# Kernel tuning notes

Hardware: AMD Instinct MI355X
Metric: run time of the kernel (lower is better)

The kernel has to match this reference:

```python
import jax, jax.numpy as jnp
import numpy as np

C, D, H, Z, B = 10, 3072, 512, 256, 2048  # classes, img_dim, hidden, latent, batch


def setup_inputs() -> dict:
    key = jax.random.key(0)
    ks = jax.random.split(key, 8)
    def w(k, shape, fan_in):
        return jax.random.normal(k, shape, jnp.float32) * (1.0 / np.sqrt(fan_in)).astype(np.float32)
    return {
        "img": jax.random.normal(ks[0], (B, D), jnp.float32),
        "label": jax.random.randint(ks[1], (B,), 0, C, dtype=jnp.int32),
        "enc_w1": w(ks[2], (C, D, H), D), "enc_b1": jnp.zeros((C, H), jnp.float32),
        "enc_w2": w(ks[3], (C, H, Z), H), "enc_b2": jnp.zeros((C, Z), jnp.float32),
        "dec_w1": w(ks[4], (C, Z, H), Z), "dec_b1": jnp.zeros((C, H), jnp.float32),
        "dec_w2": w(ks[5], (C, H, D), H), "dec_b2": jnp.zeros((C, D), jnp.float32),
    }


def reference(img, label, enc_w1, enc_b1, enc_w2, enc_b2,
              dec_w1, dec_b1, dec_w2, dec_b2):
    # Label-conditioned dispatch: rows with label==c go through expert c's
    # encoder-decoder; outputs scattered back into a zero-initialized image.
    # Loop is over a small fixed class count (structurally distinct experts);
    # masked-select via jnp.where is mathematically identical to the
    # gather/scatter in the torch code (absent classes contribute nothing).
    out_img = jnp.zeros_like(img)
    n_classes = enc_w1.shape[0]
    for c in range(n_classes):
        h = jax.nn.relu(img @ enc_w1[c] + enc_b1[c])       # [B,H]
        z = h @ enc_w2[c] + enc_b2[c]                      # [B,Z] latent code
        h2 = jax.nn.relu(z @ dec_w1[c] + dec_b1[c])        # [B,H]
        y = h2 @ dec_w2[c] + dec_b2[c]                     # [B,D]
        out_img = jnp.where((label == c)[:, None], y, out_img)
    loss = jnp.mean((out_img - img) ** 2)
    return loss, out_img
```

## Files before the change

kernel.cpp:

```cpp
#include <hip/hip_runtime.h>
#include <hip/hip_bf16.h>

#define C_CLS 10
#define DIM   3072
#define HID   512
#define LAT   256
#define BATCH 2048
#define BM    64
#define GRID_TILES 42

typedef __attribute__((ext_vector_type(8))) short  s16x8;
typedef __attribute__((ext_vector_type(4))) short  s16x4;
typedef __attribute__((ext_vector_type(4))) float  f32x4;
typedef __attribute__((ext_vector_type(8))) __bf16 bf16x8;

struct Meta {
    int offsets[C_CLS + 1];
    int ntiles;
    int tileClass[GRID_TILES];
    int tileRow[GRID_TILES];
    int perm[BATCH];
};

__device__ __forceinline__ unsigned short f2bf(float f) {
    unsigned u = __builtin_bit_cast(unsigned, f);
    unsigned r = (u + 0x7fffu + ((u >> 16) & 1u)) >> 16;
    return (unsigned short)r;
}

__device__ __forceinline__ f32x4 mfma16(s16x8 a, s16x8 b, f32x4 c) {
    return __builtin_amdgcn_mfma_f32_16x16x32_bf16(
        __builtin_bit_cast(bf16x8, a), __builtin_bit_cast(bf16x8, b), c, 0, 0, 0);
}

__global__ __launch_bounds__(256) void setup_kernel(const int* __restrict__ label,
                                                    Meta* __restrict__ mt,
                                                    float* __restrict__ out) {
    __shared__ int h[C_CLS];
    __shared__ int loff[C_CLS + 1];
    int tid = threadIdx.x;
    if (tid < C_CLS) h[tid] = 0;
    __syncthreads();
    for (int i = tid; i < BATCH; i += 256) atomicAdd(&h[label[i]], 1);
    __syncthreads();
    if (tid == 0) {
        int s = 0, nt = 0;
        for (int c = 0; c < C_CLS; ++c) { loff[c] = s; s += h[c]; }
        loff[C_CLS] = s;
        for (int c = 0; c < C_CLS; ++c) {
            mt->offsets[c] = loff[c];
            int cnt = h[c];
            for (int t = 0; t < cnt; t += BM) {
                mt->tileClass[nt] = c;
                mt->tileRow[nt]   = loff[c] + t;
                ++nt;
            }
            h[c] = loff[c];
        }
        mt->offsets[C_CLS] = loff[C_CLS];
        mt->ntiles = nt;
        out[0] = 0.0f;
    }
    __syncthreads();
    for (int i = tid; i < BATCH; i += 256) {
        int pos = atomicAdd(&h[label[i]], 1);
        mt->perm[pos] = i;
    }
}

__global__ __launch_bounds__(256) void gather_kernel(const float* __restrict__ img,
                                                     const Meta* __restrict__ mt,
                                                     unsigned short* __restrict__ Xg) {
    int p    = blockIdx.x;
    int orig = mt->perm[p];
    const float4* src = (const float4*)(img + (size_t)orig * DIM);
    unsigned short* dst = Xg + (size_t)p * DIM;
    for (int j = threadIdx.x; j < DIM / 4; j += 256) {
        float4 v = src[j];
        s16x4 o;
        o.x = (short)f2bf(v.x); o.y = (short)f2bf(v.y);
        o.z = (short)f2bf(v.z); o.w = (short)f2bf(v.w);
        *(s16x4*)(dst + 4 * j) = o;
    }
}

__global__ __launch_bounds__(256) void transpose_cvt(const float* __restrict__ src,
                                                     unsigned short* __restrict__ dst,
                                                     int K, int N) {
    __shared__ unsigned short tile[32][33];
    int c  = blockIdx.z;
    int n0 = blockIdx.x * 32, k0 = blockIdx.y * 32;
    src += (size_t)c * K * N;
    dst += (size_t)c * N * K;
    int tx = threadIdx.x, ty = threadIdx.y;
#pragma unroll
    for (int i = 0; i < 4; ++i) {
        int k = k0 + ty + i * 8;
        tile[ty + i * 8][tx] = f2bf(src[(size_t)k * N + n0 + tx]);
    }
    __syncthreads();
#pragma unroll
    for (int i = 0; i < 4; ++i) {
        int n = n0 + ty + i * 8;
        dst[(size_t)n * K + k0 + tx] = tile[tx][ty + i * 8];
    }
}

template <int K, int N, bool RELU, bool FINAL>
__global__ __launch_bounds__(256) void gemm_kernel(const unsigned short* __restrict__ A,
                                                   const unsigned short* __restrict__ Wt,
                                                   const float* __restrict__ bias,
                                                   unsigned short* __restrict__ Aout,
                                                   float* __restrict__ outF,
                                                   const float* __restrict__ img,
                                                   const Meta* __restrict__ mt) {
    int ty = blockIdx.y;
    if (ty >= mt->ntiles) return;
    const int c    = mt->tileClass[ty];
    const int r0   = mt->tileRow[ty];
    const int rend = mt->offsets[c + 1];
    const int n0   = blockIdx.x * 64;

    const unsigned short* W = Wt + ((size_t)c * N + n0) * K;

    __shared__ __align__(16) unsigned short As[64 * 64];
    __shared__ __align__(16) unsigned short Bs[64 * 64];

    const int tid  = threadIdx.x;
    const int lane = tid & 63;
    const int wid  = tid >> 6;
    const int wm   = wid >> 1, wn = wid & 1;

    f32x4 acc[2][2] = {};

    for (int k0 = 0; k0 < K; k0 += 64) {
#pragma unroll
        for (int h = 0; h < 2; ++h) {
            int ch   = tid + h * 256;
            int row  = ch >> 3;
            int slot = ch & 7;
            int ss   = slot ^ (row & 7);
            int arow = min(r0 + row, rend - 1);
            s16x8 av = *(const s16x8*)(A + (size_t)arow * K + k0 + slot * 8);
            s16x8 bv = *(const s16x8*)(W + (size_t)row * K + k0 + slot * 8);
            *(s16x8*)(As + row * 64 + ss * 8) = av;
            *(s16x8*)(Bs + row * 64 + ss * 8) = bv;
        }
        __syncthreads();
#pragma unroll
        for (int ks = 0; ks < 2; ++ks) {
            int kslot = ks * 4 + (lane >> 4);
            int rA0 = wm * 32 + (lane & 15), rA1 = rA0 + 16;
            int rB0 = wn * 32 + (lane & 15), rB1 = rB0 + 16;
            s16x8 a0 = *(const s16x8*)(As + rA0 * 64 + (kslot ^ (rA0 & 7)) * 8);
            s16x8 a1 = *(const s16x8*)(As + rA1 * 64 + (kslot ^ (rA1 & 7)) * 8);
            s16x8 b0 = *(const s16x8*)(Bs + rB0 * 64 + (kslot ^ (rB0 & 7)) * 8);
            s16x8 b1 = *(const s16x8*)(Bs + rB1 * 64 + (kslot ^ (rB1 & 7)) * 8);
            acc[0][0] = mfma16(a0, b0, acc[0][0]);
            acc[0][1] = mfma16(a0, b1, acc[0][1]);
            acc[1][0] = mfma16(a1, b0, acc[1][0]);
            acc[1][1] = mfma16(a1, b1, acc[1][1]);
        }
        __syncthreads();
    }

    const int col = lane & 15;
    const int rq  = lane >> 4;
    if constexpr (!FINAL) {
#pragma unroll
        for (int mi = 0; mi < 2; ++mi)
#pragma unroll
            for (int ni = 0; ni < 2; ++ni) {
                int n   = n0 + wn * 32 + ni * 16 + col;
                float bv = bias[(size_t)c * N + n];
#pragma unroll
                for (int r = 0; r < 4; ++r) {
                    int m = r0 + wm * 32 + mi * 16 + rq * 4 + r;
                    if (m < rend) {
                        float v = acc[mi][ni][r] + bv;
                        if (RELU) v = fmaxf(v, 0.0f);
                        Aout[(size_t)m * N + n] = f2bf(v);
                    }
                }
            }
    } else {
        float lsum = 0.0f;
#pragma unroll
        for (int mi = 0; mi < 2; ++mi) {
#pragma unroll
            for (int r = 0; r < 4; ++r) {
                int m = r0 + wm * 32 + mi * 16 + rq * 4 + r;
                if (m < rend) {
                    int orig = mt->perm[m];
#pragma unroll
                    for (int ni = 0; ni < 2; ++ni) {
                        int n   = n0 + wn * 32 + ni * 16 + col;
                        float v = acc[mi][ni][r] + bias[(size_t)c * N + n];
                        size_t idx = (size_t)orig * N + n;
                        outF[1 + idx] = v;
                        float d = v - img[idx];
                        lsum += d * d;
                    }
                }
            }
        }
#pragma unroll
        for (int o = 32; o > 0; o >>= 1) lsum += __shfl_down(lsum, o);
        __shared__ float red[4];
        if (lane == 0) red[wid] = lsum;
        __syncthreads();
        if (tid == 0)
            atomicAdd(&outF[0],
                      (red[0] + red[1] + red[2] + red[3]) * (1.0f / ((float)BATCH * (float)DIM)));
    }
}

extern "C" void kernel_launch(void* const* d_in, const int* in_sizes, int n_in,
                              void* d_out, int out_size, void* d_ws, size_t ws_size,
                              hipStream_t stream) {
    const float* img    = (const float*)d_in[0];
    const int*   label  = (const int*)d_in[1];
    const float* enc_w1 = (const float*)d_in[2];
    const float* enc_b1 = (const float*)d_in[3];
    const float* enc_w2 = (const float*)d_in[4];
    const float* enc_b2 = (const float*)d_in[5];
    const float* dec_w1 = (const float*)d_in[6];
    const float* dec_b1 = (const float*)d_in[7];
    const float* dec_w2 = (const float*)d_in[8];
    const float* dec_b2 = (const float*)d_in[9];
    float* out = (float*)d_out;

    auto alignup = [](size_t x) { return (x + 255) & ~(size_t)255; };
    char* p = (char*)d_ws;
    size_t off = 0;
    Meta* meta = (Meta*)p;                         off += alignup(sizeof(Meta));
    unsigned short* Wt1 = (unsigned short*)(p + off); off += alignup((size_t)C_CLS * HID * DIM * 2);
    unsigned short* Wt2 = (unsigned short*)(p + off); off += alignup((size_t)C_CLS * LAT * HID * 2);
    unsigned short* Wt3 = (unsigned short*)(p + off); off += alignup((size_t)C_CLS * HID * LAT * 2);
    unsigned short* Wt4 = (unsigned short*)(p + off); off += alignup((size_t)C_CLS * DIM * HID * 2);
    unsigned short* Xg  = (unsigned short*)(p + off); off += alignup((size_t)BATCH * DIM * 2);
    unsigned short* H1  = (unsigned short*)(p + off); off += alignup((size_t)BATCH * HID * 2);
    unsigned short* Z1  = (unsigned short*)(p + off); off += alignup((size_t)BATCH * LAT * 2);
    unsigned short* H2  = (unsigned short*)(p + off); off += alignup((size_t)BATCH * HID * 2);
    (void)ws_size; (void)in_sizes; (void)n_in; (void)out_size;

    setup_kernel<<<1, 256, 0, stream>>>(label, meta, out);
    gather_kernel<<<BATCH, 256, 0, stream>>>(img, meta, Xg);

    transpose_cvt<<<dim3(HID / 32, DIM / 32, C_CLS), dim3(32, 8), 0, stream>>>(enc_w1, Wt1, DIM, HID);
    transpose_cvt<<<dim3(LAT / 32, HID / 32, C_CLS), dim3(32, 8), 0, stream>>>(enc_w2, Wt2, HID, LAT);
    transpose_cvt<<<dim3(HID / 32, LAT / 32, C_CLS), dim3(32, 8), 0, stream>>>(dec_w1, Wt3, LAT, HID);
    transpose_cvt<<<dim3(DIM / 32, HID / 32, C_CLS), dim3(32, 8), 0, stream>>>(dec_w2, Wt4, HID, DIM);

    gemm_kernel<DIM, HID, true,  false><<<dim3(HID / 64, GRID_TILES), 256, 0, stream>>>(
        Xg, Wt1, enc_b1, H1, nullptr, nullptr, meta);
    gemm_kernel<HID, LAT, false, false><<<dim3(LAT / 64, GRID_TILES), 256, 0, stream>>>(
        H1, Wt2, enc_b2, Z1, nullptr, nullptr, meta);
    gemm_kernel<LAT, HID, true,  false><<<dim3(HID / 64, GRID_TILES), 256, 0, stream>>>(
        Z1, Wt3, dec_b1, H2, nullptr, nullptr, meta);
    gemm_kernel<HID, DIM, false, true ><<<dim3(DIM / 64, GRID_TILES), 256, 0, stream>>>(
        H2, Wt4, dec_b2, nullptr, out, img, meta);
}
```

Baseline: 308.4 us.

## Fuse gather and weight conversion into GEMM loads with double-buffered LDS

Removes the separate gather kernel and the four weight transpose/convert kernels. The GEMMs now read fp32 weights in their original layout and convert them to bf16 while staging into shared memory, and the first GEMM gathers image rows through the permutation directly. A two-stage shared-memory double buffer prefetches the next K tile into registers while the current one is computed. This removes several launches and the extra round trips through global memory. In exchange, each weight byte is read as fp32 (twice the bytes) by every row tile, and the conversion work is repeated per tile.

```diff
diff --git a/kernel.cpp b/kernel.cpp
--- a/kernel.cpp
+++ b/kernel.cpp
@@ -10,7 +10,6 @@
 #define GRID_TILES 42
 
 typedef __attribute__((ext_vector_type(8))) short  s16x8;
-typedef __attribute__((ext_vector_type(4))) short  s16x4;
 typedef __attribute__((ext_vector_type(4))) float  f32x4;
 typedef __attribute__((ext_vector_type(8))) __bf16 bf16x8;
 
@@ -68,47 +67,9 @@
     }
 }
 
-__global__ __launch_bounds__(256) void gather_kernel(const float* __restrict__ img,
-                                                     const Meta* __restrict__ mt,
-                                                     unsigned short* __restrict__ Xg) {
-    int p    = blockIdx.x;
-    int orig = mt->perm[p];
-    const float4* src = (const float4*)(img + (size_t)orig * DIM);
-    unsigned short* dst = Xg + (size_t)p * DIM;
-    for (int j = threadIdx.x; j < DIM / 4; j += 256) {
-        float4 v = src[j];
-        s16x4 o;
-        o.x = (short)f2bf(v.x); o.y = (short)f2bf(v.y);
-        o.z = (short)f2bf(v.z); o.w = (short)f2bf(v.w);
-        *(s16x4*)(dst + 4 * j) = o;
-    }
-}
-
-__global__ __launch_bounds__(256) void transpose_cvt(const float* __restrict__ src,
-                                                     unsigned short* __restrict__ dst,
-                                                     int K, int N) {
-    __shared__ unsigned short tile[32][33];
-    int c  = blockIdx.z;
-    int n0 = blockIdx.x * 32, k0 = blockIdx.y * 32;
-    src += (size_t)c * K * N;
-    dst += (size_t)c * N * K;
-    int tx = threadIdx.x, ty = threadIdx.y;
-#pragma unroll
-    for (int i = 0; i < 4; ++i) {
-        int k = k0 + ty + i * 8;
-        tile[ty + i * 8][tx] = f2bf(src[(size_t)k * N + n0 + tx]);
-    }
-    __syncthreads();
-#pragma unroll
-    for (int i = 0; i < 4; ++i) {
-        int n = n0 + ty + i * 8;
-        dst[(size_t)n * K + k0 + tx] = tile[tx][ty + i * 8];
-    }
-}
-
-template <int K, int N, bool RELU, bool FINAL>
-__global__ __launch_bounds__(256) void gemm_kernel(const unsigned short* __restrict__ A,
-                                                   const unsigned short* __restrict__ Wt,
+template <int K, int N, bool RELU, bool FINAL, bool GATHER>
+__global__ __launch_bounds__(256) void gemm_kernel(const void* __restrict__ Ain,
+                                                   const float* __restrict__ W,
                                                    const float* __restrict__ bias,
                                                    unsigned short* __restrict__ Aout,
                                                    float* __restrict__ outF,
@@ -121,46 +82,96 @@
     const int rend = mt->offsets[c + 1];
     const int n0   = blockIdx.x * 64;
 
-    const unsigned short* W = Wt + ((size_t)c * N + n0) * K;
-
-    __shared__ __align__(16) unsigned short As[64 * 64];
-    __shared__ __align__(16) unsigned short Bs[64 * 64];
+    const float* Wc = W + (size_t)c * K * N + n0;
+
+    __shared__ __align__(16) unsigned short As[2][64 * 64];
+    __shared__ __align__(16) unsigned short Bs[2][64 * 64];
 
     const int tid  = threadIdx.x;
     const int lane = tid & 63;
     const int wid  = tid >> 6;
     const int wm   = wid >> 1, wn = wid & 1;
 
+    const int aRow0 = tid >> 3;
+    const int aSlot = tid & 7;
+    const int bO    = tid >> 5;
+    const int bN2   = tid & 31;
+
+    float4 ga[4];
+    s16x8  aa[2];
+    float2 bb[8];
+
+    auto load_tile = [&](int k0) {
+#pragma unroll
+        for (int h = 0; h < 2; ++h) {
+            int row = aRow0 + h * 32;
+            int ar  = min(r0 + row, rend - 1);
+            if constexpr (GATHER) {
+                int orig = mt->perm[ar];
+                const float* src = (const float*)Ain + (size_t)orig * K + k0 + aSlot * 8;
+                ga[2 * h]     = *(const float4*)(src);
+                ga[2 * h + 1] = *(const float4*)(src + 4);
+            } else {
+                aa[h] = *(const s16x8*)((const unsigned short*)Ain + (size_t)ar * K + k0 + aSlot * 8);
+            }
+        }
+        const float* src = Wc + (size_t)(k0 + 8 * bO) * N + 2 * bN2;
+#pragma unroll
+        for (int i = 0; i < 8; ++i) bb[i] = *(const float2*)(src + (size_t)i * N);
+    };
+
+    auto write_tile = [&](int buf) {
+#pragma unroll
+        for (int h = 0; h < 2; ++h) {
+            int row = aRow0 + h * 32;
+            s16x8 v;
+            if constexpr (GATHER) {
+#pragma unroll
+                for (int j = 0; j < 4; ++j) {
+                    ((unsigned short*)&v)[j]     = f2bf(((const float*)&ga[2 * h])[j]);
+                    ((unsigned short*)&v)[4 + j] = f2bf(((const float*)&ga[2 * h + 1])[j]);
+                }
+            } else {
+                v = aa[h];
+            }
+            *(s16x8*)(&As[buf][row * 64 + ((aSlot ^ (row & 7))) * 8]) = v;
+        }
+#pragma unroll
+        for (int nn = 0; nn < 2; ++nn) {
+            int n = 2 * bN2 + nn;
+            s16x8 v;
+#pragma unroll
+            for (int i = 0; i < 8; ++i)
+                ((unsigned short*)&v)[i] = f2bf(nn ? bb[i].y : bb[i].x);
+            *(s16x8*)(&Bs[buf][n * 64 + ((bO ^ (n & 7))) * 8]) = v;
+        }
+    };
+
     f32x4 acc[2][2] = {};
-
-    for (int k0 = 0; k0 < K; k0 += 64) {
-#pragma unroll
-        for (int h = 0; h < 2; ++h) {
-            int ch   = tid + h * 256;
-            int row  = ch >> 3;
-            int slot = ch & 7;
-            int ss   = slot ^ (row & 7);
-            int arow = min(r0 + row, rend - 1);
-            s16x8 av = *(const s16x8*)(A + (size_t)arow * K + k0 + slot * 8);
-            s16x8 bv = *(const s16x8*)(W + (size_t)row * K + k0 + slot * 8);
-            *(s16x8*)(As + row * 64 + ss * 8) = av;
-            *(s16x8*)(Bs + row * 64 + ss * 8) = bv;
-        }
-        __syncthreads();
+    constexpr int NT = K / 64;
+
+    load_tile(0);
+    write_tile(0);
+    __syncthreads();
+
+    for (int t = 0; t < NT; ++t) {
+        int cur = t & 1;
+        if (t + 1 < NT) load_tile((t + 1) * 64);
 #pragma unroll
         for (int ks = 0; ks < 2; ++ks) {
             int kslot = ks * 4 + (lane >> 4);
             int rA0 = wm * 32 + (lane & 15), rA1 = rA0 + 16;
             int rB0 = wn * 32 + (lane & 15), rB1 = rB0 + 16;
-            s16x8 a0 = *(const s16x8*)(As + rA0 * 64 + (kslot ^ (rA0 & 7)) * 8);
-            s16x8 a1 = *(const s16x8*)(As + rA1 * 64 + (kslot ^ (rA1 & 7)) * 8);
-            s16x8 b0 = *(const s16x8*)(Bs + rB0 * 64 + (kslot ^ (rB0 & 7)) * 8);
-            s16x8 b1 = *(const s16x8*)(Bs + rB1 * 64 + (kslot ^ (rB1 & 7)) * 8);
+            s16x8 a0 = *(const s16x8*)(&As[cur][rA0 * 64 + (kslot ^ (rA0 & 7)) * 8]);
+            s16x8 a1 = *(const s16x8*)(&As[cur][rA1 * 64 + (kslot ^ (rA1 & 7)) * 8]);
+            s16x8 b0 = *(const s16x8*)(&Bs[cur][rB0 * 64 + (kslot ^ (rB0 & 7)) * 8]);
+            s16x8 b1 = *(const s16x8*)(&Bs[cur][rB1 * 64 + (kslot ^ (rB1 & 7)) * 8]);
             acc[0][0] = mfma16(a0, b0, acc[0][0]);
             acc[0][1] = mfma16(a0, b1, acc[0][1]);
             acc[1][0] = mfma16(a1, b0, acc[1][0]);
             acc[1][1] = mfma16(a1, b1, acc[1][1]);
         }
+        if (t + 1 < NT) write_tile(cur ^ 1);
         __syncthreads();
     }
 
@@ -171,7 +182,7 @@
         for (int mi = 0; mi < 2; ++mi)
 #pragma unroll
             for (int ni = 0; ni < 2; ++ni) {
-                int n   = n0 + wn * 32 + ni * 16 + col;
+                int n    = n0 + wn * 32 + ni * 16 + col;
                 float bv = bias[(size_t)c * N + n];
 #pragma unroll
                 for (int r = 0; r < 4; ++r) {
@@ -233,31 +244,20 @@
     auto alignup = [](size_t x) { return (x + 255) & ~(size_t)255; };
     char* p = (char*)d_ws;
     size_t off = 0;
-    Meta* meta = (Meta*)p;                         off += alignup(sizeof(Meta));
-    unsigned short* Wt1 = (unsigned short*)(p + off); off += alignup((size_t)C_CLS * HID * DIM * 2);
-    unsigned short* Wt2 = (unsigned short*)(p + off); off += alignup((size_t)C_CLS * LAT * HID * 2);
-    unsigned short* Wt3 = (unsigned short*)(p + off); off += alignup((size_t)C_CLS * HID * LAT * 2);
-    unsigned short* Wt4 = (unsigned short*)(p + off); off += alignup((size_t)C_CLS * DIM * HID * 2);
-    unsigned short* Xg  = (unsigned short*)(p + off); off += alignup((size_t)BATCH * DIM * 2);
-    unsigned short* H1  = (unsigned short*)(p + off); off += alignup((size_t)BATCH * HID * 2);
-    unsigned short* Z1  = (unsigned short*)(p + off); off += alignup((size_t)BATCH * LAT * 2);
-    unsigned short* H2  = (unsigned short*)(p + off); off += alignup((size_t)BATCH * HID * 2);
+    Meta* meta = (Meta*)p;                            off += alignup(sizeof(Meta));
+    unsigned short* H1 = (unsigned short*)(p + off);  off += alignup((size_t)BATCH * HID * 2);
+    unsigned short* Z1 = (unsigned short*)(p + off);  off += alignup((size_t)BATCH * LAT * 2);
+    unsigned short* H2 = (unsigned short*)(p + off);  off += alignup((size_t)BATCH * HID * 2);
     (void)ws_size; (void)in_sizes; (void)n_in; (void)out_size;
 
     setup_kernel<<<1, 256, 0, stream>>>(label, meta, out);
-    gather_kernel<<<BATCH, 256, 0, stream>>>(img, meta, Xg);
-
-    transpose_cvt<<<dim3(HID / 32, DIM / 32, C_CLS), dim3(32, 8), 0, stream>>>(enc_w1, Wt1, DIM, HID);
-    transpose_cvt<<<dim3(LAT / 32, HID / 32, C_CLS), dim3(32, 8), 0, stream>>>(enc_w2, Wt2, HID, LAT);
-    transpose_cvt<<<dim3(HID / 32, LAT / 32, C_CLS), dim3(32, 8), 0, stream>>>(dec_w1, Wt3, LAT, HID);
-    transpose_cvt<<<dim3(DIM / 32, HID / 32, C_CLS), dim3(32, 8), 0, stream>>>(dec_w2, Wt4, HID, DIM);
-
-    gemm_kernel<DIM, HID, true,  false><<<dim3(HID / 64, GRID_TILES), 256, 0, stream>>>(
-        Xg, Wt1, enc_b1, H1, nullptr, nullptr, meta);
-    gemm_kernel<HID, LAT, false, false><<<dim3(LAT / 64, GRID_TILES), 256, 0, stream>>>(
-        H1, Wt2, enc_b2, Z1, nullptr, nullptr, meta);
-    gemm_kernel<LAT, HID, true,  false><<<dim3(HID / 64, GRID_TILES), 256, 0, stream>>>(
-        Z1, Wt3, dec_b1, H2, nullptr, nullptr, meta);
-    gemm_kernel<HID, DIM, false, true ><<<dim3(DIM / 64, GRID_TILES), 256, 0, stream>>>(
-        H2, Wt4, dec_b2, nullptr, out, img, meta);
-}
+
+    gemm_kernel<DIM, HID, true,  false, true ><<<dim3(HID / 64, GRID_TILES), 256, 0, stream>>>(
+        img, enc_w1, enc_b1, H1, nullptr, nullptr, meta);
+    gemm_kernel<HID, LAT, false, false, false><<<dim3(LAT / 64, GRID_TILES), 256, 0, stream>>>(
+        H1, enc_w2, enc_b2, Z1, nullptr, nullptr, meta);
+    gemm_kernel<LAT, HID, true,  false, false><<<dim3(HID / 64, GRID_TILES), 256, 0, stream>>>(
+        Z1, dec_w1, dec_b1, H2, nullptr, nullptr, meta);
+    gemm_kernel<HID, DIM, false, true,  false><<<dim3(DIM / 64, GRID_TILES), 256, 0, stream>>>(
+        H2, dec_w2, dec_b2, nullptr, out, img, meta);
+}
```

Result: faster. 296.4 us (-3.9%).
